# Performance work log

Measured on AMD Instinct MI355X. Metric: run time of the kernel, lower is better.

## Reference

```python
import jax, jax.numpy as jnp
import numpy as np

B, T_PREV, T_CUR = 256, 128, 129
N_COV, N_TREAT, N_CONF = 30, 57, 5
H, FC = 128, 128
D_IN = N_COV + N_TREAT            # 87, lstm external input size
D_CELL = D_IN + N_CONF            # 92, cell input = [x_t, z_{t-1}]


def setup_inputs() -> dict:
    key = jax.random.key(0)
    ks = jax.random.split(key, 18)
    s = 0.05
    return {
        "previous_covariates": jax.random.normal(ks[0], (B, T_PREV, N_COV), jnp.float32),
        "previous_treatments": jax.random.normal(ks[1], (B, T_PREV, N_TREAT), jnp.float32),
        "current_covariates": jax.random.normal(ks[2], (B, T_CUR, N_COV), jnp.float32),
        "init_input": jax.random.normal(ks[3], (1, 1, D_IN), jnp.float32) * s,
        "h0": jax.random.normal(ks[4], (1, H), jnp.float32) * s,
        "c0": jax.random.normal(ks[5], (1, H), jnp.float32) * s,
        "z0": jax.random.normal(ks[6], (1, N_CONF), jnp.float32) * s,
        "W_ih": jax.random.normal(ks[7], (4 * H, D_CELL), jnp.float32) * s,
        "W_hh": jax.random.normal(ks[8], (4 * H, H), jnp.float32) * s,
        "b_ih": jax.random.normal(ks[9], (4 * H,), jnp.float32) * s,
        "b_hh": jax.random.normal(ks[10], (4 * H,), jnp.float32) * s,
        "W_z": jax.random.normal(ks[11], (N_CONF, H), jnp.float32) * s,
        "b_z": jax.random.normal(ks[12], (N_CONF,), jnp.float32) * s,
        "dec_W1": jax.random.normal(ks[13], (N_TREAT, N_COV + N_CONF, FC), jnp.float32) * s,
        "dec_b1": jax.random.normal(ks[14], (N_TREAT, FC), jnp.float32) * s,
        "dec_W2": jax.random.normal(ks[15], (N_TREAT, FC), jnp.float32) * s,
        "dec_b2": jax.random.normal(ks[16], (N_TREAT,), jnp.float32) * s,
    }


def _forward(previous_covariates, previous_treatments, current_covariates,
             init_input, h0, c0, z0, W_ih, W_hh, b_ih, b_hh, W_z, b_z,
             dec_W1, dec_b1, dec_W2, dec_b2):
    Bn = previous_covariates.shape[0]
    # (T_PREV, B, D_IN)
    x = jnp.concatenate([previous_covariates, previous_treatments], -1).transpose(1, 0, 2)
    # prepend trainable init input -> (T_CUR, B, D_IN)
    rnn_in = jnp.concatenate([jnp.broadcast_to(init_input, (1, Bn, D_IN)), x], 0)

    bias = b_ih + b_hh

    def step(carry, xt):
        h, c, z = carry
        inp = jnp.concatenate([xt, z], -1)                 # (B, D_CELL)
        gates = inp @ W_ih.T + h @ W_hh.T + bias           # (B, 4H)
        i, f, g, o = jnp.split(gates, 4, axis=-1)          # torch LSTMCell gate order
        c = jax.nn.sigmoid(f) * c + jax.nn.sigmoid(i) * jnp.tanh(g)
        h = jax.nn.sigmoid(o) * jnp.tanh(c)
        z = h @ W_z.T + b_z                                # (B, N_CONF)
        return (h, c, z), z

    carry0 = (jnp.broadcast_to(h0, (Bn, H)),
              jnp.broadcast_to(c0, (Bn, H)),
              jnp.broadcast_to(z0, (Bn, N_CONF)))
    _, zs = jax.lax.scan(step, carry0, rnn_in)             # (T_CUR, B, N_CONF)

    hidden_confounders = zs.reshape(-1, N_CONF)            # (T_CUR*B, N_CONF)
    covariates = current_covariates.transpose(1, 0, 2).reshape(-1, N_COV)
    # shapes match by construction (T_CUR*B rows each) -> no pad branch
    multitask_input = jnp.concatenate([hidden_confounders, covariates], -1)  # (N, 35)

    # batched per-treatment Linear -> LeakyReLU(0.01) -> Linear
    hdec = jax.nn.leaky_relu(
        jnp.einsum('nc,tcf->ntf', multitask_input, dec_W1) + dec_b1, 0.01)
    preds = jnp.einsum('ntf,tf->nt', hdec, dec_W2) + dec_b2                   # (N, 57)

    # T_CUR*B % (T_PREV) == 0 with these shapes -> no element trim
    confounders = hidden_confounders.reshape(T_PREV, -1, N_CONF)              # (128, 258, 5)
    return preds, confounders


def reference(previous_covariates, previous_treatments, current_covariates,
              init_input, h0, c0, z0, W_ih, W_hh, b_ih, b_hh, W_z, b_z,
              dec_W1, dec_b1, dec_W2, dec_b2):
    return _forward(previous_covariates, previous_treatments, current_covariates,
                    init_input, h0, c0, z0, W_ih, W_hh, b_ih, b_hh, W_z, b_z,
                    dec_W1, dec_b1, dec_W2, dec_b2)
```

## Files before the change

kernel.cpp:

```cpp
#include <hip/hip_runtime.h>
#include <stdint.h>

#define BATCH 256
#define T_PREVN 128
#define T_CURN 129
#define N_COV 30
#define N_TREAT 57
#define N_CONF 5
#define HID 128
#define D_IN 87
#define D_CELL 92
#define GATES 512
#define PRED_N (T_CURN*BATCH)
#define CONF_OFF (PRED_N*N_TREAT)
#define WS_NEED (57*8*2*64*8*2)
#define MT_ELEMS (PRED_N*40)
#define WS_NEED2 (WS_NEED + MT_ELEMS*2)

typedef _Float16 h2 __attribute__((ext_vector_type(2)));
typedef _Float16 h4 __attribute__((ext_vector_type(4)));
typedef _Float16 h8 __attribute__((ext_vector_type(8)));
typedef float f32x4 __attribute__((ext_vector_type(4)));

__device__ inline float rcp_fast(float x){
#if __has_builtin(__builtin_amdgcn_rcpf)
    return __builtin_amdgcn_rcpf(x);
#else
    return 1.0f / x;
#endif
}
__device__ inline float sigmoid_f(float x){ return rcp_fast(1.0f + __expf(-x)); }
__device__ inline float tanh_f(float x){ return 1.0f - 2.0f*rcp_fast(1.0f + __expf(2.0f*x)); }

__device__ inline float dot2f(h2 a, h2 b, float c){
#if __has_builtin(__builtin_amdgcn_fdot2)
    return __builtin_amdgcn_fdot2(a, b, c, false);
#else
    return c + (float)a.x*(float)b.x + (float)a.y*(float)b.y;
#endif
}
__device__ inline unsigned short f2us(float v){
    _Float16 h = (_Float16)v;
    return __builtin_bit_cast(unsigned short, h);
}
__device__ inline h2 us2h2(unsigned int u){
    return __builtin_bit_cast(h2, u);
}

__global__ __launch_bounds__(1024, 4) void lstm_scan(
    const float* __restrict__ pc, const float* __restrict__ pt,
    const float* __restrict__ init_input, const float* __restrict__ h0,
    const float* __restrict__ c0, const float* __restrict__ z0,
    const float* __restrict__ W_ih, const float* __restrict__ W_hh,
    const float* __restrict__ b_ih, const float* __restrict__ b_hh,
    const float* __restrict__ W_z, const float* __restrict__ b_z,
    float* __restrict__ zs_out, _Float16* __restrict__ mT)
{
    const int b   = blockIdx.x;
    const int tid = threadIdx.x;
    const int g   = tid >> 1;
    const int hf  = tid & 1;

    __shared__ alignas(16) unsigned short v16[224];
    __shared__ alignas(16) unsigned short xall[T_CURN*88];
    __shared__ alignas(16) unsigned short hall[T_CURN*136];
    __shared__ alignas(16) float gbuf[GATES];
    __shared__ alignas(16) _Float16 wz16[5*HID];
    __shared__ float z0c[5];

    float wzg[5];
    #pragma unroll
    for (int z = 0; z < 5; z++) wzg[z] = W_ih[g*D_CELL + 87 + z];

    float be = b_ih[g] + b_hh[g];
    #pragma unroll
    for (int z = 0; z < 5; z++) be += wzg[z] * b_z[z];

    h2 w[56];
    if (hf == 0){
        #pragma unroll
        for (int i = 0; i < 43; i++){
            h2 p; p.x = (_Float16)W_ih[g*D_CELL + 2*i];
                  p.y = (_Float16)W_ih[g*D_CELL + 2*i + 1];
            w[i] = p;
        }
        { h2 p; p.x = (_Float16)W_ih[g*D_CELL + 86]; p.y = (_Float16)0.0f; w[43] = p; }
        #pragma unroll
        for (int i = 44; i < 56; i++){
            const int u = 2*(i - 44);
            float f0 = W_hh[g*HID + u], f1 = W_hh[g*HID + u + 1];
            #pragma unroll
            for (int z = 0; z < 5; z++){
                f0 += wzg[z]*W_z[z*HID + u];
                f1 += wzg[z]*W_z[z*HID + u + 1];
            }
            h2 p; p.x = (_Float16)f0; p.y = (_Float16)f1;
            w[i] = p;
        }
    } else {
        #pragma unroll
        for (int i = 0; i < 52; i++){
            const int u = 24 + 2*i;
            float f0 = W_hh[g*HID + u], f1 = W_hh[g*HID + u + 1];
            #pragma unroll
            for (int z = 0; z < 5; z++){
                f0 += wzg[z]*W_z[z*HID + u];
                f1 += wzg[z]*W_z[z*HID + u + 1];
            }
            h2 p; p.x = (_Float16)f0; p.y = (_Float16)f1;
            w[i] = p;
        }
        #pragma unroll
        for (int i = 52; i < 56; i++){ h2 p; p.x=(_Float16)0.f; p.y=(_Float16)0.f; w[i]=p; }
    }

    for (int idx = tid; idx < T_CURN*88; idx += 1024){
        const int row = idx / 88;
        const int col = idx - row*88;
        float v = 0.0f;
        if (col < D_IN){
            if (row == 0) v = init_input[col];
            else {
                const int tp = row - 1;
                v = (col < N_COV) ? pc[(b*T_PREVN + tp)*N_COV + col]
                                  : pt[(b*T_PREVN + tp)*N_TREAT + (col - N_COV)];
            }
        }
        xall[idx] = f2us(v);
    }

    float c = 0.0f;
    if (tid < HID){ v16[88 + tid] = f2us(h0[tid]); c = c0[tid]; }
    if (tid >= 216 && tid < 224) v16[tid] = 0;

    if (tid < 5){
        float acc0 = 0.0f, acc1 = 0.0f;
        #pragma unroll 8
        for (int u = 0; u < HID; u += 2){
            acc0 += W_z[tid*HID + u]     * h0[u];
            acc1 += W_z[tid*HID + u + 1] * h0[u + 1];
        }
        z0c[tid] = z0[tid] - b_z[tid] - (acc0 + acc1);
    }
    __syncthreads();

    if (tid >= 128 && tid < 216) v16[tid - 128] = xall[tid - 128];
    float b0 = be;
    #pragma unroll
    for (int z = 0; z < 5; z++) b0 += wzg[z] * z0c[z];
    __syncthreads();

    const unsigned short* vbase = v16 + hf*112;
    for (int t = 0; t < T_CURN; t++){
        float a0 = 0.f, a1 = 0.f, a2 = 0.f, a3 = 0.f;
        #pragma unroll
        for (int i = 0; i < 14; i++){
            const uint4 q = *(const uint4*)(vbase + i*8);
            a0 = dot2f(w[4*i+0], us2h2(q.x), a0);
            a1 = dot2f(w[4*i+1], us2h2(q.y), a1);
            a2 = dot2f(w[4*i+2], us2h2(q.z), a2);
            a3 = dot2f(w[4*i+3], us2h2(q.w), a3);
        }
        float s = (a0 + a1) + (a2 + a3);
        s += __shfl_xor(s, 1);
        if (hf == 0) gbuf[g] = s + ((t == 0) ? b0 : be);
        __syncthreads();

        if (tid < HID){
            const float gi = gbuf[tid];
            const float gf = gbuf[128 + tid];
            const float gg = gbuf[256 + tid];
            const float go = gbuf[384 + tid];
            c = sigmoid_f(gf)*c + sigmoid_f(gi)*tanh_f(gg);
            const float h = sigmoid_f(go)*tanh_f(c);
            const unsigned short hu = f2us(h);
            v16[88 + tid] = hu;
            hall[t*136 + tid] = hu;
        } else if (tid < 216){
            if (t < T_PREVN) v16[tid - 128] = xall[(t + 1)*88 + (tid - 128)];
        }
        __syncthreads();
    }

    for (int i = tid; i < 5*HID; i += 1024) wz16[i] = (_Float16)W_z[i];
    __syncthreads();

    if (tid < T_CURN*N_CONF){
        const int t  = tid / 5;
        const int zi = tid - t*5;
        const uint4* hr = (const uint4*)(hall + t*136);
        const uint4* wr = (const uint4*)(wz16 + zi*HID);
        float a0 = 0.f, a1 = 0.f;
        #pragma unroll
        for (int i = 0; i < 16; i++){
            const uint4 hq = hr[i];
            const uint4 wq = wr[i];
            a0 = dot2f(us2h2(hq.x), us2h2(wq.x), a0);
            a1 = dot2f(us2h2(hq.y), us2h2(wq.y), a1);
            a0 = dot2f(us2h2(hq.z), us2h2(wq.z), a0);
            a1 = dot2f(us2h2(hq.w), us2h2(wq.w), a1);
        }
        const float z = a0 + a1 + b_z[zi];
        const int n = t*BATCH + b;
        zs_out[(size_t)n*N_CONF + zi] = z;
        if (mT) mT[(size_t)n*40 + zi] = (_Float16)z;
    }
}

__global__ __launch_bounds__(256) void prepack_w1(const float* __restrict__ dW1,
                                                  _Float16* __restrict__ wsh)
{
    const int tid = blockIdx.x*256 + threadIdx.x;
    const int treat = tid >> 10;
    const int r     = tid & 1023;
    const int ft    = r >> 7;
    const int ks    = (r >> 6) & 1;
    const int l     = r & 63;
    const int col   = ft*16 + (l & 15);
    const int kb    = ks*32 + ((l >> 4) << 3);
    h8 v;
    #pragma unroll
    for (int j = 0; j < 8; j++){
        const int k = kb + j;
        v[j] = (k < 35) ? (_Float16)dW1[(treat*35 + k)*128 + col] : (_Float16)0.0f;
    }
    *(h8*)(wsh + (size_t)tid*8) = v;
}

__global__ __launch_bounds__(256) void mt_cov(const float* __restrict__ cc,
                                              _Float16* __restrict__ mT)
{
    const int tid = blockIdx.x*256 + threadIdx.x;
    const int n = tid / 40;
    const int c = tid - n*40;
    if (c < 5) return;
    float v = 0.0f;
    if (c < 35){
        const int b = n & 255;
        const int t = n >> 8;
        v = cc[(b*T_CURN + t)*N_COV + (c - 5)];
    }
    mT[tid] = (_Float16)v;
}

__global__ __launch_bounds__(256, 2) void decoder_treat(
    const _Float16* __restrict__ mT, const _Float16* __restrict__ wsh,
    const float* __restrict__ db1, const float* __restrict__ dW2,
    const float* __restrict__ db2, float* __restrict__ preds)
{
    const int treat = blockIdx.x;
    const int rg    = blockIdx.y;
    const int w     = threadIdx.x >> 6;
    const int l     = threadIdx.x & 63;
    const int q     = l >> 4;
    const int r16   = l & 15;

    h8 bf0[8], bf1[8];
    const _Float16* bp = wsh + (size_t)treat*8192 + l*8;
    #pragma unroll
    for (int ft = 0; ft < 8; ft++){
        bf0[ft] = *(const h8*)(bp + ft*1024);
        bf1[ft] = *(const h8*)(bp + ft*1024 + 512);
    }
    float b1r[8], w2r[8], w2c[8];
    #pragma unroll
    for (int ft = 0; ft < 8; ft++){
        b1r[ft] = db1[treat*128 + ft*16 + r16];
        w2r[ft] = dW2[treat*128 + ft*16 + r16];
        w2c[ft] = 0.01f * w2r[ft];
    }
    const float b2 = db2[treat];

    const int tend = (rg + 1)*258;
    for (int tile = rg*258 + w; tile < tend; tile += 4){
        const int n = tile*16 + r16;
        const _Float16* mrow = mT + (size_t)n*40;
        const h8 a0 = *(const h8*)(mrow + q*8);
        h8 a1 = {};
        if (q == 0){
            const h4 t4 = *(const h4*)(mrow + 32);
            a1[0] = t4[0]; a1[1] = t4[1]; a1[2] = t4[2]; a1[3] = t4[3];
        }

        f32x4 pred = {0.f, 0.f, 0.f, 0.f};
        #pragma unroll
        for (int ft = 0; ft < 8; ft++){
            f32x4 acc = {b1r[ft], b1r[ft], b1r[ft], b1r[ft]};
            acc = __builtin_amdgcn_mfma_f32_16x16x32_f16(a0, bf0[ft], acc, 0, 0, 0);
            acc = __builtin_amdgcn_mfma_f32_16x16x32_f16(a1, bf1[ft], acc, 0, 0, 0);
            #pragma unroll
            for (int r = 0; r < 4; r++){
                const float a  = acc[r];
                const float mx = fmaxf(a, 0.0f);
                const float mn = fminf(a, 0.0f);
                pred[r] += mx*w2r[ft] + mn*w2c[ft];
            }
        }
        #pragma unroll
        for (int r = 0; r < 4; r++){
            float s = pred[r];
            s += __shfl_xor(s, 1);
            s += __shfl_xor(s, 2);
            s += __shfl_xor(s, 4);
            s += __shfl_xor(s, 8);
            pred[r] = s;
        }
        if (r16 == 0){
            #pragma unroll
            for (int r = 0; r < 4; r++)
                preds[(size_t)(tile*16 + q*4 + r)*N_TREAT + treat] = pred[r] + b2;
        }
    }
}

__global__ __launch_bounds__(256) void decoder_mfma(
    const float* __restrict__ cc, const float* __restrict__ zs,
    const _Float16* __restrict__ wsh,
    const float* __restrict__ db1, const float* __restrict__ dW2,
    const float* __restrict__ db2, float* __restrict__ preds)
{
    __shared__ alignas(16) _Float16 m_lds[64*72];

    const int tid  = threadIdx.x;
    const int base = blockIdx.x * 64;
    const int t    = base >> 8;

    for (int idx = tid; idx < 64*72; idx += 256){
        const int r = idx / 72;
        const int j = idx - r*72;
        const int n = base + r;
        const int b = n & 255;
        float v = 0.0f;
        if (j < 5)       v = zs[n*N_CONF + j];
        else if (j < 35) v = cc[(b*T_CURN + t)*N_COV + (j - 5)];
        m_lds[r*72 + j] = (_Float16)v;
    }
    __syncthreads();

    const int w    = tid >> 6;
    const int l    = tid & 63;
    const int row  = l & 15;
    const int quad = l >> 4;

    const _Float16* arow = m_lds + (w*16 + row)*72 + quad*8;
    const h8 a0 = *(const h8*)(arow);
    const h8 a1 = *(const h8*)(arow + 32);
    const int nbase = base + w*16 + quad*4;

    for (int treat = 0; treat < 57; treat++){
        const _Float16* bp = wsh + (size_t)treat*8192 + l*8;
        f32x4 pred = {0.0f, 0.0f, 0.0f, 0.0f};
        #pragma unroll
        for (int ft = 0; ft < 8; ft++){
            const h8 b0 = *(const h8*)(bp + ft*1024);
            const h8 b1 = *(const h8*)(bp + ft*1024 + 512);
            f32x4 acc = {0.0f, 0.0f, 0.0f, 0.0f};
            acc = __builtin_amdgcn_mfma_f32_16x16x32_f16(a0, b0, acc, 0, 0, 0);
            acc = __builtin_amdgcn_mfma_f32_16x16x32_f16(a1, b1, acc, 0, 0, 0);
            const int col = ft*16 + row;
            const float hb1 = db1[treat*128 + col];
            const float hw2 = dW2[treat*128 + col];
            #pragma unroll
            for (int r = 0; r < 4; r++){
                float hd = acc[r] + hb1;
                hd = (hd > 0.0f) ? hd : 0.01f*hd;
                pred[r] += hd * hw2;
            }
        }
        #pragma unroll
        for (int r = 0; r < 4; r++){
            float s = pred[r];
            s += __shfl_xor(s, 1);
            s += __shfl_xor(s, 2);
            s += __shfl_xor(s, 4);
            s += __shfl_xor(s, 8);
            pred[r] = s;
        }
        if (row == 0){
            const float b2 = db2[treat];
            #pragma unroll
            for (int r = 0; r < 4; r++)
                preds[(size_t)(nbase + r)*N_TREAT + treat] = pred[r] + b2;
        }
    }
}

__global__ __launch_bounds__(256) void decoder_fallback(
    const float* __restrict__ cc, const float* __restrict__ zs,
    const float* __restrict__ dW1, const float* __restrict__ db1,
    const float* __restrict__ dW2, const float* __restrict__ db2,
    float* __restrict__ preds)
{
    const int t     = blockIdx.x;
    const int treat = blockIdx.y;
    const int tid   = threadIdx.x;

    __shared__ alignas(16) float w1t[128*36];
    __shared__ float b1s[128];
    __shared__ float w2s[128];

    for (int it = tid; it < 35*128; it += 256){
        const int cidx = it >> 7;
        const int f    = it & 127;
        w1t[f*36 + cidx] = dW1[(treat*35 + cidx)*128 + f];
    }
    if (tid < 128){
        b1s[tid] = db1[treat*128 + tid];
        w2s[tid] = dW2[treat*128 + tid];
        w1t[tid*36 + 35] = 0.0f;
    }
    __syncthreads();

    const int n = t*BATCH + tid;
    float m[36];
    #pragma unroll
    for (int j = 0; j < N_CONF; j++) m[j] = zs[n*N_CONF + j];
    #pragma unroll
    for (int j = 0; j < N_COV; j++)  m[N_CONF + j] = cc[(tid*T_CURN + t)*N_COV + j];
    m[35] = 0.0f;

    const float b2 = db2[treat];
    float pred = 0.0f;
    for (int f = 0; f < 128; f++){
        float a = b1s[f];
        const float4* wr = (const float4*)(w1t + f*36);
        #pragma unroll
        for (int cq = 0; cq < 9; cq++){
            const float4 v = wr[cq];
            a += m[cq*4+0]*v.x + m[cq*4+1]*v.y + m[cq*4+2]*v.z + m[cq*4+3]*v.w;
        }
        a = (a > 0.0f) ? a : 0.01f*a;
        pred += a * w2s[f];
    }
    preds[n*N_TREAT + treat] = pred + b2;
}

extern "C" void kernel_launch(void* const* d_in, const int* in_sizes, int n_in,
                              void* d_out, int out_size, void* d_ws, size_t ws_size,
                              hipStream_t stream)
{
    const float* pc   = (const float*)d_in[0];
    const float* pt   = (const float*)d_in[1];
    const float* cc   = (const float*)d_in[2];
    const float* init = (const float*)d_in[3];
    const float* h0   = (const float*)d_in[4];
    const float* c0   = (const float*)d_in[5];
    const float* z0   = (const float*)d_in[6];
    const float* W_ih = (const float*)d_in[7];
    const float* W_hh = (const float*)d_in[8];
    const float* b_ih = (const float*)d_in[9];
    const float* b_hh = (const float*)d_in[10];
    const float* W_z  = (const float*)d_in[11];
    const float* b_z  = (const float*)d_in[12];
    const float* dW1  = (const float*)d_in[13];
    const float* db1  = (const float*)d_in[14];
    const float* dW2  = (const float*)d_in[15];
    const float* db2  = (const float*)d_in[16];

    float* preds = (float*)d_out;
    float* zs    = (float*)d_out + CONF_OFF;

    const bool ws_full = (ws_size >= (size_t)WS_NEED2);
    const bool ws_w1   = (ws_size >= (size_t)WS_NEED);

    _Float16* wsh = (_Float16*)d_ws;
    _Float16* mT  = (_Float16*)((char*)d_ws + WS_NEED);

    if (ws_w1)
        prepack_w1<<<228, 256, 0, stream>>>(dW1, wsh);
    if (ws_full)
        mt_cov<<<5160, 256, 0, stream>>>(cc, mT);

    lstm_scan<<<BATCH, 1024, 0, stream>>>(pc, pt, init, h0, c0, z0,
                                          W_ih, W_hh, b_ih, b_hh, W_z, b_z,
                                          zs, ws_full ? mT : (_Float16*)nullptr);

    if (ws_full)
        decoder_treat<<<dim3(N_TREAT, 8), 256, 0, stream>>>(mT, wsh, db1, dW2, db2, preds);
    else if (ws_w1)
        decoder_mfma<<<516, 256, 0, stream>>>(cc, zs, wsh, db1, dW2, db2, preds);
    else
        decoder_fallback<<<dim3(T_CURN, N_TREAT), 256, 0, stream>>>(
            cc, zs, dW1, db1, dW2, db2, preds);
}
```

Measured before the change: 224.3 us.

## Hoist LSTM input projection into a batched MFMA GEMM and fold z into W_hh

Precomputes the input-to-gate projection for all timesteps with an MFMA GEMM (gx_gemm) into an fp16 workspace buffer. The scan kernel then only does the recurrent matvec and streams in precomputed Gx rows with double buffering. It also folds the z feedback path algebraically into W_hh and the bias (z = W_z h + b_z), which removes the per-step z computation. This adds a large fp16 workspace buffer and more launches. It is only used when the workspace is big enough, and fp16 Gx plus folded weights may cost accuracy.

```diff
diff --git a/kernel.cpp b/kernel.cpp
--- a/kernel.cpp
+++ b/kernel.cpp
@@ -13,9 +13,18 @@
 #define GATES 512
 #define PRED_N (T_CURN*BATCH)
 #define CONF_OFF (PRED_N*N_TREAT)
-#define WS_NEED (57*8*2*64*8*2)
-#define MT_ELEMS (PRED_N*40)
-#define WS_NEED2 (WS_NEED + MT_ELEMS*2)
+
+#define OFF_W1   0
+#define SZ_W1    (57*8*2*64*8*2)
+#define OFF_WIH  SZ_W1
+#define SZ_WIH   (32*3*64*8*2)
+#define OFF_GX   (OFF_W1 + SZ_W1 + SZ_WIH)
+#define SZ_GX    (PRED_N*512*2)
+#define OFF_MT   (OFF_GX + SZ_GX)
+#define SZ_MT    (PRED_N*40*2)
+#define WS_GX    (OFF_MT + SZ_MT)
+#define WS_NEED  SZ_W1
+#define WS_NEED2 (SZ_W1 + SZ_MT)
 
 typedef _Float16 h2 __attribute__((ext_vector_type(2)));
 typedef _Float16 h4 __attribute__((ext_vector_type(4)));
@@ -47,7 +56,241 @@
     return __builtin_bit_cast(h2, u);
 }
 
-__global__ __launch_bounds__(1024, 4) void lstm_scan(
+__global__ __launch_bounds__(256) void prepack_wih(const float* __restrict__ W_ih,
+                                                   _Float16* __restrict__ wihf)
+{
+    const int tid = blockIdx.x*256 + threadIdx.x;
+    const int ct  = tid / 192;
+    const int rem = tid - ct*192;
+    const int ks  = rem >> 6;
+    const int l   = rem & 63;
+    const int gate = ct*16 + (l & 15);
+    const int kb   = ks*32 + ((l >> 4) << 3);
+    h8 v;
+    #pragma unroll
+    for (int j = 0; j < 8; j++){
+        const int k = kb + j;
+        v[j] = (k < D_IN) ? (_Float16)W_ih[gate*D_CELL + k] : (_Float16)0.0f;
+    }
+    *(h8*)(wihf + (size_t)tid*8) = v;
+}
+
+__global__ __launch_bounds__(256, 2) void gx_gemm(
+    const float* __restrict__ pc, const float* __restrict__ pt,
+    const float* __restrict__ init_input,
+    const _Float16* __restrict__ wihf, _Float16* __restrict__ Gx)
+{
+    __shared__ alignas(16) _Float16 a_lds[64*104];
+    __shared__ alignas(16) _Float16 gx_lds[64*264];
+
+    const int tid = threadIdx.x;
+    const int nb  = blockIdx.x * 64;
+
+    for (int idx = tid; idx < 64*96; idx += 256){
+        const int r = idx / 96;
+        const int k = idx - r*96;
+        const int n = nb + r;
+        const int bb = n / 129;
+        const int t  = n - bb*129;
+        float v = 0.0f;
+        if (k < D_IN){
+            if (t == 0) v = init_input[k];
+            else        v = (k < N_COV) ? pc[(bb*T_PREVN + t-1)*N_COV + k]
+                                        : pt[(bb*T_PREVN + t-1)*N_TREAT + (k - N_COV)];
+        }
+        a_lds[r*104 + k] = (_Float16)v;
+    }
+    __syncthreads();
+
+    const int w    = tid >> 6;
+    const int l    = tid & 63;
+    const int col  = l & 15;
+    const int quad = l >> 4;
+
+    const _Float16* ar = a_lds + (w*16 + col)*104 + quad*8;
+    const h8 a0 = *(const h8*)(ar);
+    const h8 a1 = *(const h8*)(ar + 32);
+    const h8 a2 = *(const h8*)(ar + 64);
+
+    for (int half = 0; half < 2; half++){
+        #pragma unroll
+        for (int ct8 = 0; ct8 < 16; ct8++){
+            const int ct = half*16 + ct8;
+            const _Float16* bp = wihf + (size_t)ct*1536 + l*8;
+            const h8 b0 = *(const h8*)(bp);
+            const h8 b1 = *(const h8*)(bp + 512);
+            const h8 b2 = *(const h8*)(bp + 1024);
+            f32x4 acc = {0.f, 0.f, 0.f, 0.f};
+            acc = __builtin_amdgcn_mfma_f32_16x16x32_f16(a0, b0, acc, 0, 0, 0);
+            acc = __builtin_amdgcn_mfma_f32_16x16x32_f16(a1, b1, acc, 0, 0, 0);
+            acc = __builtin_amdgcn_mfma_f32_16x16x32_f16(a2, b2, acc, 0, 0, 0);
+            #pragma unroll
+            for (int r4 = 0; r4 < 4; r4++)
+                gx_lds[(w*16 + quad*4 + r4)*264 + ct8*16 + col] = (_Float16)acc[r4];
+        }
+        __syncthreads();
+        #pragma unroll
+        for (int it = 0; it < 8; it++){
+            const int idx = it*256 + tid;
+            const int r   = idx >> 5;
+            const int seg = idx & 31;
+            *(h8*)(Gx + ((size_t)(nb + r))*512 + half*256 + seg*8) =
+                *(const h8*)(&gx_lds[r*264 + seg*8]);
+        }
+        __syncthreads();
+    }
+}
+
+__global__ __launch_bounds__(1024, 4) void lstm_scan_gx(
+    const float* __restrict__ h0, const float* __restrict__ c0,
+    const float* __restrict__ z0,
+    const float* __restrict__ W_ih, const float* __restrict__ W_hh,
+    const float* __restrict__ b_ih, const float* __restrict__ b_hh,
+    const float* __restrict__ W_z, const float* __restrict__ b_z,
+    const _Float16* __restrict__ Gx,
+    float* __restrict__ zs_out, _Float16* __restrict__ mT)
+{
+    const int b   = blockIdx.x;
+    const int tid = threadIdx.x;
+    const int grp = tid >> 2;
+    const int j   = tid & 3;
+    const int g0  = grp*2, g1 = g0 + 1;
+
+    __shared__ alignas(16) unsigned short v16h[128];
+    __shared__ alignas(16) unsigned short hall[T_CURN*136];
+    __shared__ alignas(16) float gbuf[GATES];
+    __shared__ alignas(16) unsigned short gxbuf[2][512];
+    __shared__ alignas(16) _Float16 wz16[5*HID];
+    __shared__ alignas(16) float wzf[5*HID];
+    __shared__ float z0c[5];
+
+    for (int i = tid; i < 5*HID; i += 1024) wzf[i] = W_z[i];
+
+    float c = 0.0f;
+    if (tid < HID){ v16h[tid] = f2us(h0[tid]); c = c0[tid]; }
+
+    if (tid < 5){
+        float acc0 = 0.0f, acc1 = 0.0f;
+        #pragma unroll 8
+        for (int u = 0; u < HID; u += 2){
+            acc0 += W_z[tid*HID + u]     * h0[u];
+            acc1 += W_z[tid*HID + u + 1] * h0[u + 1];
+        }
+        z0c[tid] = z0[tid] - b_z[tid] - (acc0 + acc1);
+    }
+    if (tid >= 960){
+        const int lane = tid - 960;
+        const uint4 q = *(const uint4*)(Gx + ((size_t)b*T_CURN)*512 + lane*8);
+        *(uint4*)(&gxbuf[0][lane*8]) = q;
+    }
+    __syncthreads();
+
+    float wz0[5], wz1[5];
+    #pragma unroll
+    for (int z = 0; z < 5; z++){
+        wz0[z] = W_ih[g0*D_CELL + D_IN + z];
+        wz1[z] = W_ih[g1*D_CELL + D_IN + z];
+    }
+    float be0 = b_ih[g0] + b_hh[g0];
+    float be1 = b_ih[g1] + b_hh[g1];
+    #pragma unroll
+    for (int z = 0; z < 5; z++){ be0 += wz0[z]*b_z[z]; be1 += wz1[z]*b_z[z]; }
+
+    h2 w0[16], w1[16];
+    {
+        const int kb = j*32;
+        #pragma unroll
+        for (int i = 0; i < 16; i++){
+            const int k = kb + 2*i;
+            float f00 = W_hh[g0*HID + k],     f01 = W_hh[g0*HID + k + 1];
+            float f10 = W_hh[g1*HID + k],     f11 = W_hh[g1*HID + k + 1];
+            #pragma unroll
+            for (int z = 0; z < 5; z++){
+                const float a = wzf[z*HID + k], bb2 = wzf[z*HID + k + 1];
+                f00 += wz0[z]*a;  f01 += wz0[z]*bb2;
+                f10 += wz1[z]*a;  f11 += wz1[z]*bb2;
+            }
+            h2 p0; p0.x = (_Float16)f00; p0.y = (_Float16)f01; w0[i] = p0;
+            h2 p1; p1.x = (_Float16)f10; p1.y = (_Float16)f11; w1[i] = p1;
+        }
+    }
+    float b00 = be0, b01 = be1;
+    #pragma unroll
+    for (int z = 0; z < 5; z++){ b00 += wz0[z]*z0c[z]; b01 += wz1[z]*z0c[z]; }
+
+    const unsigned short* vb = v16h + j*32;
+    for (int t = 0; t < T_CURN; t++){
+        uint4 pre;
+        if (tid >= 960 && t < T_CURN-1)
+            pre = *(const uint4*)(Gx + ((size_t)b*T_CURN + t + 1)*512 + (tid-960)*8);
+
+        float s0a=0.f, s0b=0.f, s1a=0.f, s1b=0.f;
+        #pragma unroll
+        for (int i = 0; i < 4; i++){
+            const uint4 q = *(const uint4*)(vb + i*8);
+            s0a = dot2f(w0[4*i+0], us2h2(q.x), s0a);
+            s0b = dot2f(w0[4*i+1], us2h2(q.y), s0b);
+            s0a = dot2f(w0[4*i+2], us2h2(q.z), s0a);
+            s0b = dot2f(w0[4*i+3], us2h2(q.w), s0b);
+            s1a = dot2f(w1[4*i+0], us2h2(q.x), s1a);
+            s1b = dot2f(w1[4*i+1], us2h2(q.y), s1b);
+            s1a = dot2f(w1[4*i+2], us2h2(q.z), s1a);
+            s1b = dot2f(w1[4*i+3], us2h2(q.w), s1b);
+        }
+        float s0 = s0a + s0b, s1 = s1a + s1b;
+        s0 += __shfl_xor(s0, 1);  s0 += __shfl_xor(s0, 2);
+        s1 += __shfl_xor(s1, 1);  s1 += __shfl_xor(s1, 2);
+        if (j == 0){
+            const h2 gx = us2h2(*(const unsigned int*)(&gxbuf[t & 1][g0]));
+            float2 gg;
+            gg.x = s0 + (float)gx.x + ((t == 0) ? b00 : be0);
+            gg.y = s1 + (float)gx.y + ((t == 0) ? b01 : be1);
+            *(float2*)(&gbuf[g0]) = gg;
+        }
+        __syncthreads();
+
+        if (tid < HID){
+            const float gi = gbuf[tid];
+            const float gf = gbuf[128 + tid];
+            const float gg = gbuf[256 + tid];
+            const float go = gbuf[384 + tid];
+            c = sigmoid_f(gf)*c + sigmoid_f(gi)*tanh_f(gg);
+            const float h = sigmoid_f(go)*tanh_f(c);
+            const unsigned short hu = f2us(h);
+            v16h[tid] = hu;
+            hall[t*136 + tid] = hu;
+        } else if (tid >= 960 && t < T_CURN-1){
+            *(uint4*)(&gxbuf[(t+1) & 1][(tid-960)*8]) = pre;
+        }
+        __syncthreads();
+    }
+
+    for (int i = tid; i < 5*HID; i += 1024) wz16[i] = (_Float16)W_z[i];
+    __syncthreads();
+
+    if (tid < T_CURN*N_CONF){
+        const int t  = tid / 5;
+        const int zi = tid - t*5;
+        const uint4* hr = (const uint4*)(hall + t*136);
+        const uint4* wr = (const uint4*)(wz16 + zi*HID);
+        float a0 = 0.f, a1 = 0.f;
+        #pragma unroll
+        for (int i = 0; i < 16; i++){
+            const uint4 hq = hr[i];
+            const uint4 wq = wr[i];
+            a0 = dot2f(us2h2(hq.x), us2h2(wq.x), a0);
+            a1 = dot2f(us2h2(hq.y), us2h2(wq.y), a1);
+            a0 = dot2f(us2h2(hq.z), us2h2(wq.z), a0);
+            a1 = dot2f(us2h2(hq.w), us2h2(wq.w), a1);
+        }
+        const float z = a0 + a1 + b_z[zi];
+        const int n = t*BATCH + b;
+        zs_out[(size_t)n*N_CONF + zi] = z;
+        if (mT) mT[(size_t)n*40 + zi] = (_Float16)z;
+    }
+}
+
+__global__ __launch_bounds__(1024, 4) void lstm_scan_old(
     const float* __restrict__ pc, const float* __restrict__ pt,
     const float* __restrict__ init_input, const float* __restrict__ h0,
     const float* __restrict__ c0, const float* __restrict__ z0,
@@ -460,26 +703,39 @@
     float* preds = (float*)d_out;
     float* zs    = (float*)d_out + CONF_OFF;
 
-    const bool ws_full = (ws_size >= (size_t)WS_NEED2);
-    const bool ws_w1   = (ws_size >= (size_t)WS_NEED);
-
-    _Float16* wsh = (_Float16*)d_ws;
-    _Float16* mT  = (_Float16*)((char*)d_ws + WS_NEED);
-
-    if (ws_w1)
+    if (ws_size >= (size_t)WS_GX){
+        _Float16* wsh  = (_Float16*)d_ws;
+        _Float16* wihf = (_Float16*)((char*)d_ws + OFF_WIH);
+        _Float16* Gx   = (_Float16*)((char*)d_ws + OFF_GX);
+        _Float16* mT   = (_Float16*)((char*)d_ws + OFF_MT);
+
         prepack_w1<<<228, 256, 0, stream>>>(dW1, wsh);
-    if (ws_full)
+        prepack_wih<<<24, 256, 0, stream>>>(W_ih, wihf);
         mt_cov<<<5160, 256, 0, stream>>>(cc, mT);
-
-    lstm_scan<<<BATCH, 1024, 0, stream>>>(pc, pt, init, h0, c0, z0,
-                                          W_ih, W_hh, b_ih, b_hh, W_z, b_z,
-                                          zs, ws_full ? mT : (_Float16*)nullptr);
-
-    if (ws_full)
+        gx_gemm<<<516, 256, 0, stream>>>(pc, pt, init, wihf, Gx);
+        lstm_scan_gx<<<BATCH, 1024, 0, stream>>>(h0, c0, z0, W_ih, W_hh,
+                                                 b_ih, b_hh, W_z, b_z, Gx, zs, mT);
         decoder_treat<<<dim3(N_TREAT, 8), 256, 0, stream>>>(mT, wsh, db1, dW2, db2, preds);
-    else if (ws_w1)
+    } else if (ws_size >= (size_t)WS_NEED2){
+        _Float16* wsh = (_Float16*)d_ws;
+        _Float16* mT  = (_Float16*)((char*)d_ws + WS_NEED);
+        prepack_w1<<<228, 256, 0, stream>>>(dW1, wsh);
+        mt_cov<<<5160, 256, 0, stream>>>(cc, mT);
+        lstm_scan_old<<<BATCH, 1024, 0, stream>>>(pc, pt, init, h0, c0, z0,
+                                                  W_ih, W_hh, b_ih, b_hh, W_z, b_z, zs, mT);
+        decoder_treat<<<dim3(N_TREAT, 8), 256, 0, stream>>>(mT, wsh, db1, dW2, db2, preds);
+    } else if (ws_size >= (size_t)WS_NEED){
+        _Float16* wsh = (_Float16*)d_ws;
+        prepack_w1<<<228, 256, 0, stream>>>(dW1, wsh);
+        lstm_scan_old<<<BATCH, 1024, 0, stream>>>(pc, pt, init, h0, c0, z0,
+                                                  W_ih, W_hh, b_ih, b_hh, W_z, b_z,
+                                                  zs, (_Float16*)nullptr);
         decoder_mfma<<<516, 256, 0, stream>>>(cc, zs, wsh, db1, dW2, db2, preds);
-    else
+    } else {
+        lstm_scan_old<<<BATCH, 1024, 0, stream>>>(pc, pt, init, h0, c0, z0,
+                                                  W_ih, W_hh, b_ih, b_hh, W_z, b_z,
+                                                  zs, (_Float16*)nullptr);
         decoder_fallback<<<dim3(T_CURN, N_TREAT), 256, 0, stream>>>(
             cc, zs, dW1, db1, dW2, db2, preds);
-}
+    }
+}
```

Result: slower. 267.4 us (+19.2%).
